# Kernel optimization log

Hardware: AMD Instinct MI355X
Metric: run time of the kernel (lower is better)

## Reference

```python
import jax, jax.numpy as jnp
import numpy as np

NEG_SLOPE = 0.2
EPS = 1e-12


def setup_inputs() -> dict:
    key = jax.random.key(0)
    k1, k2, k3, k4, k5 = jax.random.split(key, 5)
    N, E, IN, OUT = 100000, 1600000, 256, 64
    x = jax.random.normal(k1, (N, IN), dtype=jnp.float32)
    edge_index = jax.random.randint(k2, (2, E), 0, N, dtype=jnp.int64)
    # GATConv (heads=1) parameters: lin weight, att_src, att_dst, bias
    W = jax.random.normal(k3, (IN, OUT), dtype=jnp.float32) * (1.0 / np.sqrt(IN))
    att_src = jax.random.normal(k4, (OUT,), dtype=jnp.float32) * (1.0 / np.sqrt(OUT))
    att_dst = jax.random.normal(k5, (OUT,), dtype=jnp.float32) * (1.0 / np.sqrt(OUT))
    bias = jnp.zeros((OUT,), dtype=jnp.float32)
    return {"x": x, "edge_index": edge_index, "W": W,
            "att_src": att_src, "att_dst": att_dst, "bias": bias}


def reference(x, edge_index, W, att_src, att_dst, bias):
    N = x.shape[0]
    # PyG GATConv default add_self_loops=True
    loops = jnp.arange(N, dtype=edge_index.dtype)
    src = jnp.concatenate([edge_index[0], loops])  # source j of edge (j -> i)
    dst = jnp.concatenate([edge_index[1], loops])  # target i (softmax segment)

    h = x @ W                                      # [N, out]
    a_src = h @ att_src                            # [N] per-node source score
    a_dst = h @ att_dst                            # [N] per-node target score

    e = jax.nn.leaky_relu(a_src[src] + a_dst[dst], NEG_SLOPE)  # [E+N]
    # segment softmax over incoming edges of each destination node
    e_max = jax.ops.segment_max(e, dst, num_segments=N)
    e = jnp.exp(e - e_max[dst])
    denom = jax.ops.segment_sum(e, dst, num_segments=N)
    alpha = e / denom[dst]                         # [E+N]

    # scatter-aggregate: out[i] = sum_j alpha_ij * h[j]
    out = jax.ops.segment_sum(alpha[:, None] * h[src], dst, num_segments=N)
    out = out + bias

    # dropout (p=0.3) in eval mode is identity; then F.normalize (row-wise L2)
    nrm = jnp.sqrt(jnp.sum(out * out, axis=-1, keepdims=True))
    return out / jnp.maximum(nrm, EPS)
```

## Files before the change

kernel.cpp:

```cpp
#include <hip/hip_runtime.h>
#include <hip/hip_bf16.h>
#include <math.h>

#define NEG_SLOPE 0.2f
#define EPS_NRM 1e-12f
#define K_IN 256
#define C_OUT 64
#define BK 32
#define ROWS_PB 128

__global__ __launch_bounds__(256) void gemm_att(
    const float* __restrict__ x, const float* __restrict__ W,
    const float* __restrict__ att_s, const float* __restrict__ att_d,
    __hip_bfloat16* __restrict__ h, float* __restrict__ a_src_arr,
    float* __restrict__ a_dst_arr, int N,
    const int* __restrict__ dstA, int* __restrict__ cnt, int E)
{
    __shared__ float xt[BK][ROWS_PB];
    __shared__ float wt[BK][C_OUT];

    int t  = threadIdx.x;
    int tx = t & 15;
    int ty = t >> 4;
    int row0 = blockIdx.x * ROWS_PB;

    int sr  = t >> 1;
    int skh = (t & 1) * 16;
    int srow = row0 + sr; if (srow >= N) srow = N - 1;
    const float* xsp = x + (size_t)srow * K_IN + skh;

    float acc[8][4];
#pragma unroll
    for (int r = 0; r < 8; ++r)
#pragma unroll
        for (int c = 0; c < 4; ++c) acc[r][c] = 0.f;

    for (int k0 = 0; k0 < K_IN; k0 += BK) {
        float4 xa = *(const float4*)(xsp + k0);
        float4 xb = *(const float4*)(xsp + k0 + 4);
        float4 xc = *(const float4*)(xsp + k0 + 8);
        float4 xd = *(const float4*)(xsp + k0 + 12);
        float4 wv4a = *(const float4*)(W + (size_t)k0 * C_OUT + t * 4);
        float4 wv4b = *(const float4*)(W + (size_t)(k0 + 16) * C_OUT + t * 4);
        __syncthreads();
        xt[skh +  0][sr] = xa.x; xt[skh +  1][sr] = xa.y;
        xt[skh +  2][sr] = xa.z; xt[skh +  3][sr] = xa.w;
        xt[skh +  4][sr] = xb.x; xt[skh +  5][sr] = xb.y;
        xt[skh +  6][sr] = xb.z; xt[skh +  7][sr] = xb.w;
        xt[skh +  8][sr] = xc.x; xt[skh +  9][sr] = xc.y;
        xt[skh + 10][sr] = xc.z; xt[skh + 11][sr] = xc.w;
        xt[skh + 12][sr] = xd.x; xt[skh + 13][sr] = xd.y;
        xt[skh + 14][sr] = xd.z; xt[skh + 15][sr] = xd.w;
        *(float4*)(&wt[ 0][0] + t * 4) = wv4a;
        *(float4*)(&wt[16][0] + t * 4) = wv4b;
        __syncthreads();

#pragma unroll
        for (int k = 0; k < BK; ++k) {
            float xv[8];
            *(float4*)&xv[0] = *(const float4*)&xt[k][ty * 8];
            *(float4*)&xv[4] = *(const float4*)&xt[k][ty * 8 + 4];
            float4 wv = *(const float4*)&wt[k][tx * 4];
#pragma unroll
            for (int r = 0; r < 8; ++r) {
                acc[r][0] += xv[r] * wv.x;
                acc[r][1] += xv[r] * wv.y;
                acc[r][2] += xv[r] * wv.z;
                acc[r][3] += xv[r] * wv.w;
            }
        }
    }

    float4 avl = *(const float4*)(att_s + tx * 4);
    float4 dvl = *(const float4*)(att_d + tx * 4);
#pragma unroll
    for (int r = 0; r < 8; ++r) {
        int row = row0 + ty * 8 + r;
        if (row >= N) continue;
        float ps = acc[r][0] * avl.x + acc[r][1] * avl.y +
                   acc[r][2] * avl.z + acc[r][3] * avl.w;
        float pd = acc[r][0] * dvl.x + acc[r][1] * dvl.y +
                   acc[r][2] * dvl.z + acc[r][3] * dvl.w;
#pragma unroll
        for (int d = 1; d < 16; d <<= 1) {
            ps += __shfl_xor(ps, d, 64);
            pd += __shfl_xor(pd, d, 64);
        }
        if (tx == 0) { a_src_arr[row] = ps; a_dst_arr[row] = pd; }
        __hip_bfloat16 hb[4];
#pragma unroll
        for (int c = 0; c < 4; ++c) hb[c] = __float2bfloat16(acc[r][c]);
        *(ushort2*)(h + (size_t)row * C_OUT + tx * 4) =
            make_ushort2(*(unsigned short*)&hb[0], *(unsigned short*)&hb[1]);
        *(ushort2*)(h + (size_t)row * C_OUT + tx * 4 + 2) =
            make_ushort2(*(unsigned short*)&hb[2], *(unsigned short*)&hb[3]);
    }

    int stride = gridDim.x * blockDim.x;
    for (int i = blockIdx.x * blockDim.x + t; i < E; i += stride)
        atomicAdd(&cnt[dstA[i]], 1);
}

__global__ __launch_bounds__(256) void scan_p1(
    const int* __restrict__ cnt, int* __restrict__ partials, int n)
{
    int b = blockIdx.x, t = threadIdx.x;
    int base = b * 1024;
    int s = 0;
#pragma unroll
    for (int j = 0; j < 4; ++j) {
        int i = base + t * 4 + j;
        if (i < n) s += cnt[i];
    }
    for (int d = 1; d < 64; d <<= 1) s += __shfl_xor(s, d, 64);
    __shared__ int wsum[4];
    int lane = t & 63, wid = t >> 6;
    if (lane == 0) wsum[wid] = s;
    __syncthreads();
    if (t == 0) partials[b] = wsum[0] + wsum[1] + wsum[2] + wsum[3];
}

__global__ __launch_bounds__(256) void scan_p2(int* partials, int nb)
{
    __shared__ int buf[256];
    int t = threadIdx.x;
    int v = (t < nb) ? partials[t] : 0;
    buf[t] = v;
    __syncthreads();
    for (int d = 1; d < 256; d <<= 1) {
        int w = (t >= d) ? buf[t - d] : 0;
        __syncthreads();
        buf[t] += w;
        __syncthreads();
    }
    if (t < nb) partials[t] = buf[t] - v;
}

__global__ __launch_bounds__(256) void scan_p3(
    const int* __restrict__ cnt, const int* __restrict__ partials,
    int* __restrict__ offsets, int n)
{
    int b = blockIdx.x, t = threadIdx.x;
    int base = b * 1024;
    int v[4];
    int s = 0;
#pragma unroll
    for (int j = 0; j < 4; ++j) {
        int i = base + t * 4 + j;
        v[j] = (i < n) ? cnt[i] : 0;
        s += v[j];
    }
    int lane = t & 63, wid = t >> 6;
    int incl = s;
    for (int d = 1; d < 64; d <<= 1) {
        int w = __shfl_up(incl, d, 64);
        if (lane >= d) incl += w;
    }
    __shared__ int wsum[4];
    __shared__ int wbase[4];
    if (lane == 63) wsum[wid] = incl;
    __syncthreads();
    if (t == 0) {
        int r = 0;
        for (int i = 0; i < 4; ++i) { wbase[i] = r; r += wsum[i]; }
    }
    __syncthreads();
    int run = partials[b] + wbase[wid] + (incl - s);
#pragma unroll
    for (int j = 0; j < 4; ++j) {
        int i = base + t * 4 + j;
        if (i < n) {
            offsets[i] = run;
            run += v[j];
            if (i == n - 1) offsets[n] = run;
        }
    }
}

__global__ __launch_bounds__(256) void scatter_edges(
    const int* __restrict__ srcA, const int* __restrict__ dstA,
    const int* __restrict__ offsets, int* __restrict__ cursor,
    const float* __restrict__ a_src, const float* __restrict__ a_dst,
    unsigned long long* __restrict__ csr, int E)
{
    int i = blockIdx.x * blockDim.x + threadIdx.x;
    if (i >= E) return;
    int s = srcA[i], d = dstA[i];
    float e = a_src[s] + a_dst[d];
    e = fmaxf(e, NEG_SLOPE * e);
    float w = __expf(e);
    int pos = offsets[d] + atomicAdd(&cursor[d], 1);
    unsigned long long packed =
        (unsigned long long)(unsigned)s |
        ((unsigned long long)__float_as_uint(w) << 32);
    __builtin_nontemporal_store(packed, &csr[pos]);
}

__global__ __launch_bounds__(256) void gat_pull(
    const int* __restrict__ offsets, const int2* __restrict__ csr,
    const unsigned short* __restrict__ h, const float* __restrict__ a_src,
    const float* __restrict__ a_dst, const float* __restrict__ bias,
    float* __restrict__ out, int N)
{
    int gw   = (blockIdx.x * blockDim.x + threadIdx.x) >> 6;
    int lane = threadIdx.x & 63;
    int grp  = lane >> 4;
    int gl   = lane & 15;
    int node = gw * 4 + grp;
    bool valid = node < N;
    int nv = valid ? node : 0;

    int beg = offsets[nv];
    int n   = valid ? (offsets[nv + 1] - beg) : 0;
    const int2* ce = csr + (n ? beg : 0);

    float asv = a_src[nv], adv = a_dst[nv];
    float es = asv + adv; es = fmaxf(es, NEG_SLOPE * es);
    float ws = __expf(es);
    unsigned long long hu = *(const unsigned long long*)
        (h + (size_t)nv * C_OUT + 4 * gl);
    unsigned hl = (unsigned)hu, hh = (unsigned)(hu >> 32);
    float acc0 = ws * __uint_as_float(hl << 16);
    float acc1 = ws * __uint_as_float(hl & 0xffff0000u);
    float acc2 = ws * __uint_as_float(hh << 16);
    float acc3 = ws * __uint_as_float(hh & 0xffff0000u);
    float den = ws;

    int2 c0 = ce[0];
    int2 c1 = ce[(n > 1) ? 1 : 0];
    unsigned long long u0 = *(const unsigned long long*)
        (h + (size_t)c0.x * C_OUT + 4 * gl);
    unsigned long long u1 = *(const unsigned long long*)
        (h + (size_t)c1.x * C_OUT + 4 * gl);

    for (int p = 0; p < n; p += 2) {
        int2 m0 = ce[(p + 2 < n) ? p + 2 : 0];
        int2 m1 = ce[(p + 3 < n) ? p + 3 : 0];
        unsigned long long v0 = *(const unsigned long long*)
            (h + (size_t)m0.x * C_OUT + 4 * gl);
        unsigned long long v1 = *(const unsigned long long*)
            (h + (size_t)m1.x * C_OUT + 4 * gl);

        float w0 = __int_as_float(c0.y);
        float w1 = (p + 1 < n) ? __int_as_float(c1.y) : 0.f;
        unsigned l0 = (unsigned)u0, h0 = (unsigned)(u0 >> 32);
        unsigned l1 = (unsigned)u1, h1 = (unsigned)(u1 >> 32);
        den  += w0 + w1;
        acc0 += w0 * __uint_as_float(l0 << 16)
              + w1 * __uint_as_float(l1 << 16);
        acc1 += w0 * __uint_as_float(l0 & 0xffff0000u)
              + w1 * __uint_as_float(l1 & 0xffff0000u);
        acc2 += w0 * __uint_as_float(h0 << 16)
              + w1 * __uint_as_float(h1 << 16);
        acc3 += w0 * __uint_as_float(h0 & 0xffff0000u)
              + w1 * __uint_as_float(h1 & 0xffff0000u);

        c0 = m0; c1 = m1; u0 = v0; u1 = v1;
    }

    float4 bl = *(const float4*)(bias + 4 * gl);
    float rd = 1.f / den;
    float o0 = acc0 * rd + bl.x;
    float o1 = acc1 * rd + bl.y;
    float o2 = acc2 * rd + bl.z;
    float o3 = acc3 * rd + bl.w;

    float sq = o0 * o0 + o1 * o1 + o2 * o2 + o3 * o3;
#pragma unroll
    for (int d = 1; d < 16; d <<= 1) sq += __shfl_xor(sq, d, 64);
    float rn = 1.f / fmaxf(sqrtf(sq), EPS_NRM);

    if (valid)
        *(float4*)(out + (size_t)node * C_OUT + 4 * gl) =
            make_float4(o0 * rn, o1 * rn, o2 * rn, o3 * rn);
}

extern "C" void kernel_launch(void* const* d_in, const int* in_sizes, int n_in,
                              void* d_out, int out_size, void* d_ws, size_t ws_size,
                              hipStream_t stream)
{
    const float* x     = (const float*)d_in[0];
    const int*   ei    = (const int*)d_in[1];
    const float* W     = (const float*)d_in[2];
    const float* att_s = (const float*)d_in[3];
    const float* att_d = (const float*)d_in[4];
    const float* bias  = (const float*)d_in[5];
    float*       out   = (float*)d_out;

    const int OUT = in_sizes[3];
    const int IN  = in_sizes[2] / OUT;
    const int N   = in_sizes[0] / IN;
    const int E   = in_sizes[1] / 2;

    char* w = (char*)d_ws;
    auto alloc = [&](size_t bytes) -> void* {
        void* p = (void*)w;
        w += (bytes + 255) & ~(size_t)255;
        return p;
    };
    __hip_bfloat16* h = (__hip_bfloat16*)alloc((size_t)N * C_OUT * 2);
    float* a_src  = (float*)alloc((size_t)N * 4);
    float* a_dst  = (float*)alloc((size_t)N * 4);
    int*   cnt    = (int*)alloc((size_t)N * 2 * 4);
    int*   offs   = (int*)alloc((size_t)(N + 1) * 4);
    int*   parts  = (int*)alloc(1024 * 4);
    unsigned long long* csr = (unsigned long long*)alloc((size_t)E * 8);
    int*   cursor = cnt + N;

    hipMemsetAsync(cnt, 0, (size_t)N * 2 * 4, stream);

    gemm_att<<<(N + ROWS_PB - 1) / ROWS_PB, 256, 0, stream>>>(
        x, W, att_s, att_d, h, a_src, a_dst, N, ei + E, cnt, E);

    int NB = (N + 1023) / 1024;
    scan_p1<<<NB, 256, 0, stream>>>(cnt, parts, N);
    scan_p2<<<1, 256, 0, stream>>>(parts, NB);
    scan_p3<<<NB, 256, 0, stream>>>(cnt, parts, offs, N);

    scatter_edges<<<(E + 255) / 256, 256, 0, stream>>>(
        ei, ei + E, offs, cursor, a_src, a_dst, csr, E);

    gat_pull<<<(N + 15) / 16, 256, 0, stream>>>(offs, (const int2*)csr,
        (const unsigned short*)h, a_src, a_dst, bias, out, N);
}
```

Baseline: 367.5 us.

## Double-buffer GEMM tiles with row-major padded x tile and smaller row tile

Rewrites the x@W projection kernel to use 64-row tiles with double-buffered shared memory. The next K-slice's global loads are issued before computing on the current slice, and only one barrier is used per step. The x tile is now stored row-major with padding instead of as a transposed scalar scatter, which avoids bank-conflicting transpose stores. Each thread now computes a 4x4 output tile instead of 8x4, doubling the grid, which adds block overhead and lowers per-thread arithmetic intensity.

```diff
diff --git a/kernel.cpp b/kernel.cpp
--- a/kernel.cpp
+++ b/kernel.cpp
@@ -7,7 +7,8 @@
 #define K_IN 256
 #define C_OUT 64
 #define BK 32
-#define ROWS_PB 128
+#define TILE_M 64
+#define XPAD 36
 
 __global__ __launch_bounds__(256) void gemm_att(
     const float* __restrict__ x, const float* __restrict__ W,
@@ -16,67 +17,84 @@
     float* __restrict__ a_dst_arr, int N,
     const int* __restrict__ dstA, int* __restrict__ cnt, int E)
 {
-    __shared__ float xt[BK][ROWS_PB];
-    __shared__ float wt[BK][C_OUT];
+    __shared__ float xs[2][TILE_M][XPAD];
+    __shared__ float ws[2][BK][C_OUT];
 
     int t  = threadIdx.x;
     int tx = t & 15;
     int ty = t >> 4;
-    int row0 = blockIdx.x * ROWS_PB;
-
-    int sr  = t >> 1;
-    int skh = (t & 1) * 16;
-    int srow = row0 + sr; if (srow >= N) srow = N - 1;
-    const float* xsp = x + (size_t)srow * K_IN + skh;
-
-    float acc[8][4];
-#pragma unroll
-    for (int r = 0; r < 8; ++r)
+    int row0 = blockIdx.x * TILE_M;
+
+    int xr  = t >> 2;
+    int xko = (t & 3) * 8;
+    int srow = row0 + xr; if (srow >= N) srow = N - 1;
+    const float* xp = x + (size_t)srow * K_IN + xko;
+
+    int wkr = t >> 3;
+    int wco = (t & 7) * 8;
+    const float* wp = W + (size_t)wkr * C_OUT + wco;
+
+    float acc[4][4];
+#pragma unroll
+    for (int r = 0; r < 4; ++r)
 #pragma unroll
         for (int c = 0; c < 4; ++c) acc[r][c] = 0.f;
 
+    float4 xA = *(const float4*)(xp);
+    float4 xB = *(const float4*)(xp + 4);
+    float4 wA = *(const float4*)(wp);
+    float4 wB = *(const float4*)(wp + 4);
+    *(float4*)&xs[0][xr][xko]       = xA;
+    *(float4*)&xs[0][xr][xko + 4]   = xB;
+    *(float4*)&ws[0][wkr][wco]      = wA;
+    *(float4*)&ws[0][wkr][wco + 4]  = wB;
+    __syncthreads();
+
+    int buf = 0;
     for (int k0 = 0; k0 < K_IN; k0 += BK) {
-        float4 xa = *(const float4*)(xsp + k0);
-        float4 xb = *(const float4*)(xsp + k0 + 4);
-        float4 xc = *(const float4*)(xsp + k0 + 8);
-        float4 xd = *(const float4*)(xsp + k0 + 12);
-        float4 wv4a = *(const float4*)(W + (size_t)k0 * C_OUT + t * 4);
-        float4 wv4b = *(const float4*)(W + (size_t)(k0 + 16) * C_OUT + t * 4);
-        __syncthreads();
-        xt[skh +  0][sr] = xa.x; xt[skh +  1][sr] = xa.y;
-        xt[skh +  2][sr] = xa.z; xt[skh +  3][sr] = xa.w;
-        xt[skh +  4][sr] = xb.x; xt[skh +  5][sr] = xb.y;
-        xt[skh +  6][sr] = xb.z; xt[skh +  7][sr] = xb.w;
-        xt[skh +  8][sr] = xc.x; xt[skh +  9][sr] = xc.y;
-        xt[skh + 10][sr] = xc.z; xt[skh + 11][sr] = xc.w;
-        xt[skh + 12][sr] = xd.x; xt[skh + 13][sr] = xd.y;
-        xt[skh + 14][sr] = xd.z; xt[skh + 15][sr] = xd.w;
-        *(float4*)(&wt[ 0][0] + t * 4) = wv4a;
-        *(float4*)(&wt[16][0] + t * 4) = wv4b;
-        __syncthreads();
-
-#pragma unroll
-        for (int k = 0; k < BK; ++k) {
-            float xv[8];
-            *(float4*)&xv[0] = *(const float4*)&xt[k][ty * 8];
-            *(float4*)&xv[4] = *(const float4*)&xt[k][ty * 8 + 4];
-            float4 wv = *(const float4*)&wt[k][tx * 4];
-#pragma unroll
-            for (int r = 0; r < 8; ++r) {
-                acc[r][0] += xv[r] * wv.x;
-                acc[r][1] += xv[r] * wv.y;
-                acc[r][2] += xv[r] * wv.z;
-                acc[r][3] += xv[r] * wv.w;
+        const bool more = (k0 + BK) < K_IN;
+        if (more) {
+            xA = *(const float4*)(xp + k0 + BK);
+            xB = *(const float4*)(xp + k0 + BK + 4);
+            wA = *(const float4*)(wp + (size_t)(k0 + BK) * C_OUT);
+            wB = *(const float4*)(wp + (size_t)(k0 + BK) * C_OUT + 4);
+        }
+
+#pragma unroll
+        for (int kk = 0; kk < BK; kk += 4) {
+            float xq[4][4];
+            *(float4*)xq[0] = *(const float4*)&xs[buf][ty * 4 + 0][kk];
+            *(float4*)xq[1] = *(const float4*)&xs[buf][ty * 4 + 1][kk];
+            *(float4*)xq[2] = *(const float4*)&xs[buf][ty * 4 + 2][kk];
+            *(float4*)xq[3] = *(const float4*)&xs[buf][ty * 4 + 3][kk];
+#pragma unroll
+            for (int j = 0; j < 4; ++j) {
+                float4 wv = *(const float4*)&ws[buf][kk + j][tx * 4];
+#pragma unroll
+                for (int r = 0; r < 4; ++r) {
+                    acc[r][0] += xq[r][j] * wv.x;
+                    acc[r][1] += xq[r][j] * wv.y;
+                    acc[r][2] += xq[r][j] * wv.z;
+                    acc[r][3] += xq[r][j] * wv.w;
+                }
             }
+        }
+
+        if (more) {
+            *(float4*)&xs[buf ^ 1][xr][xko]      = xA;
+            *(float4*)&xs[buf ^ 1][xr][xko + 4]  = xB;
+            *(float4*)&ws[buf ^ 1][wkr][wco]     = wA;
+            *(float4*)&ws[buf ^ 1][wkr][wco + 4] = wB;
+            __syncthreads();
+            buf ^= 1;
         }
     }
 
     float4 avl = *(const float4*)(att_s + tx * 4);
     float4 dvl = *(const float4*)(att_d + tx * 4);
 #pragma unroll
-    for (int r = 0; r < 8; ++r) {
-        int row = row0 + ty * 8 + r;
-        if (row >= N) continue;
+    for (int r = 0; r < 4; ++r) {
+        int row = row0 + ty * 4 + r;
         float ps = acc[r][0] * avl.x + acc[r][1] * avl.y +
                    acc[r][2] * avl.z + acc[r][3] * avl.w;
         float pd = acc[r][0] * dvl.x + acc[r][1] * dvl.y +
@@ -86,14 +104,16 @@
             ps += __shfl_xor(ps, d, 64);
             pd += __shfl_xor(pd, d, 64);
         }
-        if (tx == 0) { a_src_arr[row] = ps; a_dst_arr[row] = pd; }
-        __hip_bfloat16 hb[4];
-#pragma unroll
-        for (int c = 0; c < 4; ++c) hb[c] = __float2bfloat16(acc[r][c]);
-        *(ushort2*)(h + (size_t)row * C_OUT + tx * 4) =
-            make_ushort2(*(unsigned short*)&hb[0], *(unsigned short*)&hb[1]);
-        *(ushort2*)(h + (size_t)row * C_OUT + tx * 4 + 2) =
-            make_ushort2(*(unsigned short*)&hb[2], *(unsigned short*)&hb[3]);
+        if (row < N) {
+            if (tx == 0) { a_src_arr[row] = ps; a_dst_arr[row] = pd; }
+            __hip_bfloat16 hb[4];
+#pragma unroll
+            for (int c = 0; c < 4; ++c) hb[c] = __float2bfloat16(acc[r][c]);
+            *(ushort2*)(h + (size_t)row * C_OUT + tx * 4) =
+                make_ushort2(*(unsigned short*)&hb[0], *(unsigned short*)&hb[1]);
+            *(ushort2*)(h + (size_t)row * C_OUT + tx * 4 + 2) =
+                make_ushort2(*(unsigned short*)&hb[2], *(unsigned short*)&hb[3]);
+        }
     }
 
     int stride = gridDim.x * blockDim.x;
@@ -309,7 +329,7 @@
 
     hipMemsetAsync(cnt, 0, (size_t)N * 2 * 4, stream);
 
-    gemm_att<<<(N + ROWS_PB - 1) / ROWS_PB, 256, 0, stream>>>(
+    gemm_att<<<(N + TILE_M - 1) / TILE_M, 256, 0, stream>>>(
         x, W, att_s, att_d, h, a_src, a_dst, N, ei + E, cnt, E);
 
     int NB = (N + 1023) / 1024;
```

Measured after the change: 352.5 us. 1.04x faster.
